# Performance work log

Measured on AMD Instinct MI355X. Metric: run time of the kernel, lower is better.

Reference implementation:

```python
import jax, jax.numpy as jnp
import numpy as np

B = 1024       # repertoires (batch)
TCR = 100      # instances (TCRs) per repertoire
FEAT = 15      # feature_num (conv in_channels)
AA = 24        # aa_num (sequence length)
KS = [2, 3, 4, 5, 6, 7]
FN = [3, 3, 3, 2, 2, 1]
NINP = 14      # sum(FN)
EPS = 1e-5     # BatchNorm eps


def sparsemax(z):
    # z: (B, K); sparsemax along axis 1 (Martins & Astudillo 2016)
    K = z.shape[1]
    zs = -jnp.sort(-z, axis=1)               # descending sort
    cs = jnp.cumsum(zs, axis=1)
    k = jnp.arange(1, K + 1, dtype=z.dtype)
    support = 1.0 + k * zs > cs              # (B, K) bool
    ksel = jnp.sum(support, axis=1, keepdims=True).astype(jnp.int32)  # support size
    tau = (jnp.take_along_axis(cs, ksel - 1, axis=1) - 1.0) / ksel.astype(z.dtype)
    return jnp.maximum(z - tau, 0.0)


def setup_inputs() -> dict:
    key = jax.random.key(0)
    ks = jax.random.split(key, 12)
    inp = {"x": jax.random.normal(ks[0], (B, TCR, FEAT, AA), dtype=jnp.float32)}
    for i, (h, f) in enumerate(zip(KS, FN)):
        inp[f"cw{i}"] = jax.random.normal(ks[1 + i], (f, FEAT, h), dtype=jnp.float32) * 0.1
        inp[f"cb{i}"] = jnp.zeros((f,), dtype=jnp.float32)
    inp["fc1_w"] = jax.random.normal(ks[7], (NINP, NINP), dtype=jnp.float32) * 0.2
    inp["fc1_b"] = jnp.zeros((NINP,), dtype=jnp.float32)
    inp["waout_w"] = jax.random.normal(ks[8], (1, NINP), dtype=jnp.float32) * 0.2
    inp["decf_w"] = jax.random.normal(ks[9], (NINP, NINP), dtype=jnp.float32) * 0.2
    inp["decf_b"] = jnp.zeros((NINP,), dtype=jnp.float32)
    inp["bn_g"] = jnp.ones((NINP,), dtype=jnp.float32)
    inp["bn_b"] = jnp.zeros((NINP,), dtype=jnp.float32)
    inp["decs_w"] = jax.random.normal(ks[10], (2, NINP), dtype=jnp.float32) * 0.2
    inp["decs_b"] = jnp.zeros((2,), dtype=jnp.float32)
    return inp


def reference(x, cw0, cb0, cw1, cb1, cw2, cb2, cw3, cb3, cw4, cb4, cw5, cb5,
              fc1_w, fc1_b, waout_w, decf_w, decf_b, bn_g, bn_b, decs_w, decs_b):
    xf = x.reshape(-1, FEAT, AA)  # (B*TCR, 15, 24)
    feats = []
    for w, b in ((cw0, cb0), (cw1, cb1), (cw2, cb2), (cw3, cb3), (cw4, cb4), (cw5, cb5)):
        y = jax.lax.conv_general_dilated(xf, w, (1,), 'VALID',
                                         dimension_numbers=('NCH', 'OIH', 'NCH'))
        y = jax.nn.relu(y + b[None, :, None])
        feats.append(jnp.max(y, axis=-1))  # AdaptiveMaxPool1d(1): global max over length
    out = jnp.concatenate(feats, axis=1).reshape(-1, TCR, NINP)  # (B, TCR, 14)
    # fclayer1 + dropout(eval=identity) + relu; applied per-instance so the
    # torch (TCR, B, .) transpose is equivalent to working in (B, TCR, .)
    h = jax.nn.relu(out @ fc1_w.T + fc1_b)                       # (B, TCR, 14)
    attw = sparsemax(h @ waout_w[0])                             # (B, TCR)
    pooled = jnp.einsum('bt,btd->bd', attw, h)                   # bmm(attw[:,None,:], h)
    z = pooled @ decf_w.T + decf_b                               # decoder_f
    mu = jnp.mean(z, axis=0)                                     # BatchNorm1d (batch stats)
    var = jnp.var(z, axis=0)
    z = jax.nn.relu((z - mu) / jnp.sqrt(var + EPS) * bn_g + bn_b)
    logits = z @ decs_w.T + decs_b                               # decoder_s -> (B, 2)
    return logits, attw
```

## Files before the change

kernel.cpp:

```cpp
#include <hip/hip_runtime.h>

typedef unsigned int  u32;
typedef unsigned short u16;

__device__ __forceinline__ float bf2f(u16 u){
    return __uint_as_float(((u32)u) << 16);
}
__device__ __forceinline__ float lo16(u32 v){ return __uint_as_float(v << 16); }
__device__ __forceinline__ float hi16(u32 v){ return __uint_as_float(v & 0xffff0000u); }
__device__ __forceinline__ u16 f2bf(float f){
    u32 x = __float_as_uint(f);
    x += 0x7fffu + ((x >> 16) & 1u);
    return (u16)(x >> 16);
}
__device__ __forceinline__ float ldany(const void* p, int i, bool bf){
    return bf ? bf2f(((const u16*)p)[i]) : ((const float*)p)[i];
}

#define B_      1024
#define TCR_    100
#define NINST   (B_*TCR_)

#define OFF_WCH    0
#define OFF_CB     840
#define OFF_FC1W   854
#define OFF_FC1B   1050
#define OFF_WA     1064
#define OFF_DECFW  1078
#define OFF_DECFB  1274
#define OFF_BNG    1288
#define OFF_BNB    1302
#define OFF_DECSW  1316
#define OFF_DECSB  1344

__global__ __launch_bounds__(256) void k_pack(
    const void* cw0, const void* cb0, const void* cw1, const void* cb1,
    const void* cw2, const void* cb2, const void* cw3, const void* cb3,
    const void* cw4, const void* cb4, const void* cw5, const void* cb5,
    const void* fc1_w, const void* fc1_b, const void* waout,
    const void* decf_w, const void* decf_b,
    const void* bn_g, const void* bn_b,
    const void* decs_w, const void* decs_b,
    float* __restrict__ wsP)
{
    const int tid = threadIdx.x;
    const bool bf = (((const u16*)bn_g)[0] == 0x3F80u);

    for (int widx = tid; widx < 840; widx += 256){
        float val; int dst;
        if (widx < 90)      { int e = widx;       int c=e/6,  rr=e-c*6,  ff=rr/2, j=rr-ff*2; val=ldany(cw0,(ff*15+c)*2+j,bf); dst=c*56+ 0+ff*2+j; }
        else if (widx < 225){ int e = widx - 90;  int c=e/9,  rr=e-c*9,  ff=rr/3, j=rr-ff*3; val=ldany(cw1,(ff*15+c)*3+j,bf); dst=c*56+ 6+ff*3+j; }
        else if (widx < 405){ int e = widx - 225; int c=e/12, rr=e-c*12, ff=rr/4, j=rr-ff*4; val=ldany(cw2,(ff*15+c)*4+j,bf); dst=c*56+15+ff*4+j; }
        else if (widx < 555){ int e = widx - 405; int c=e/10, rr=e-c*10, ff=rr/5, j=rr-ff*5; val=ldany(cw3,(ff*15+c)*5+j,bf); dst=c*56+27+ff*5+j; }
        else if (widx < 735){ int e = widx - 555; int c=e/12, rr=e-c*12, ff=rr/6, j=rr-ff*6; val=ldany(cw4,(ff*15+c)*6+j,bf); dst=c*56+37+ff*6+j; }
        else                { int e = widx - 735; int c=e/7,  j=e-c*7;                        val=ldany(cw5,c*7+j,bf);        dst=c*56+49+j; }
        wsP[OFF_WCH + dst] = val;
    }
    for (int i = tid; i < 14; i += 256){
        float bv;
        if (i < 3)       bv = ldany(cb0, i, bf);
        else if (i < 6)  bv = ldany(cb1, i - 3, bf);
        else if (i < 9)  bv = ldany(cb2, i - 6, bf);
        else if (i < 11) bv = ldany(cb3, i - 9, bf);
        else if (i < 13) bv = ldany(cb4, i - 11, bf);
        else             bv = ldany(cb5, 0, bf);
        wsP[OFF_CB    + i] = bv;
        wsP[OFF_FC1B  + i] = ldany(fc1_b,  i, bf);
        wsP[OFF_WA    + i] = ldany(waout,  i, bf);
        wsP[OFF_DECFB + i] = ldany(decf_b, i, bf);
        wsP[OFF_BNG   + i] = ldany(bn_g,   i, bf);
        wsP[OFF_BNB   + i] = ldany(bn_b,   i, bf);
    }
    for (int i = tid; i < 196; i += 256){
        wsP[OFF_FC1W  + i] = ldany(fc1_w,  i, bf);
        wsP[OFF_DECFW + i] = ldany(decf_w, i, bf);
    }
    for (int i = tid; i < 28; i += 256) wsP[OFF_DECSW + i] = ldany(decs_w, i, bf);
    for (int i = tid; i < 2;  i += 256) wsP[OFF_DECSB + i] = ldany(decs_b, i, bf);
}

template<int H, int F, int GOFF>
__device__ __forceinline__ void acc_ch(float (&acc)[F][17 - H], const float* xr,
                                       const float* __restrict__ wch){
    float wv[F * H];
    #pragma unroll
    for (int k = 0; k < F * H; ++k) wv[k] = wch[GOFF + k];
    #pragma unroll
    for (int ff = 0; ff < F; ++ff)
        #pragma unroll
        for (int i = 0; i < 17 - H; ++i)
            #pragma unroll
            for (int j = 0; j < H; ++j)
                acc[ff][i] = fmaf(wv[ff * H + j], xr[i + j], acc[ff][i]);
}

template<int H, int F, int OF>
__device__ __forceinline__ void pair_max(float (&acc)[F][17 - H],
                                         const float* __restrict__ wsP, float* feats){
    #pragma unroll
    for (int ff = 0; ff < F; ++ff){
        float m = acc[ff][0];
        #pragma unroll
        for (int i = 1; i < 17 - H; ++i) m = fmaxf(m, acc[ff][i]);
        m = fmaxf(m, __shfl_xor(m, 1));
        feats[OF + ff] = fmaxf(m + wsP[OFF_CB + OF + ff], 0.0f);
    }
}

template<bool BF>
__device__ __forceinline__ void unpack16(const uint4* buf, float* xr){
    if (BF){
        #pragma unroll
        for (int i = 0; i < 2; ++i){
            u32 w0 = buf[i].x, w1 = buf[i].y, w2 = buf[i].z, w3 = buf[i].w;
            xr[i*8+0] = lo16(w0); xr[i*8+1] = hi16(w0);
            xr[i*8+2] = lo16(w1); xr[i*8+3] = hi16(w1);
            xr[i*8+4] = lo16(w2); xr[i*8+5] = hi16(w2);
            xr[i*8+6] = lo16(w3); xr[i*8+7] = hi16(w3);
        }
    } else {
        #pragma unroll
        for (int i = 0; i < 4; ++i){
            xr[i*4+0] = __uint_as_float(buf[i].x);
            xr[i*4+1] = __uint_as_float(buf[i].y);
            xr[i*4+2] = __uint_as_float(buf[i].z);
            xr[i*4+3] = __uint_as_float(buf[i].w);
        }
    }
}

template<bool BF>
__device__ __forceinline__ void conv_body(const void* __restrict__ x,
                                          const float* __restrict__ wsP,
                                          float* __restrict__ hbufT,
                                          float* __restrict__ sbuf){
    constexpr int NB = BF ? 2 : 4;
    constexpr int CS = BF ? 48 : 96;
    const int tid   = threadIdx.x;
    const int tpart = tid & 1;
    const int inst  = blockIdx.x * 128 + (tid >> 1);
    const char* xb  = (const char*)x + (size_t)inst * (BF ? 720 : 1440)
                                     + tpart * (BF ? 16 : 32);

    float a2[3][15], a3[3][14], a4[3][13], a5[2][12], a6[2][11], a7[1][10];
    #pragma unroll
    for (int f = 0; f < 3; ++f){
        #pragma unroll
        for (int i = 0; i < 15; ++i) a2[f][i] = 0.0f;
        #pragma unroll
        for (int i = 0; i < 14; ++i) a3[f][i] = 0.0f;
        #pragma unroll
        for (int i = 0; i < 13; ++i) a4[f][i] = 0.0f;
    }
    #pragma unroll
    for (int f = 0; f < 2; ++f){
        #pragma unroll
        for (int i = 0; i < 12; ++i) a5[f][i] = 0.0f;
        #pragma unroll
        for (int i = 0; i < 11; ++i) a6[f][i] = 0.0f;
    }
    #pragma unroll
    for (int i = 0; i < 10; ++i) a7[0][i] = 0.0f;

    uint4 cur[NB];
    {
        const uint4* p = (const uint4*)xb;
        #pragma unroll
        for (int i = 0; i < NB; ++i) cur[i] = p[i];
    }
    #pragma unroll 1
    for (int c = 0; c < 15; ++c){
        uint4 nxt[NB];
        int cn = (c < 14) ? (c + 1) : 14;
        const uint4* pn = (const uint4*)(xb + cn * CS);
        #pragma unroll
        for (int i = 0; i < NB; ++i) nxt[i] = pn[i];

        float xr[16];
        unpack16<BF>(cur, xr);
        const float* wch = wsP + OFF_WCH + c * 56;
        acc_ch<2,3, 0>(a2, xr, wch);
        acc_ch<3,3, 6>(a3, xr, wch);
        acc_ch<4,3,15>(a4, xr, wch);
        acc_ch<5,2,27>(a5, xr, wch);
        acc_ch<6,2,37>(a6, xr, wch);
        acc_ch<7,1,49>(a7, xr, wch);

        #pragma unroll
        for (int i = 0; i < NB; ++i) cur[i] = nxt[i];
    }

    float feats[14];
    pair_max<2,3, 0>(a2, wsP, feats);
    pair_max<3,3, 3>(a3, wsP, feats);
    pair_max<4,3, 6>(a4, wsP, feats);
    pair_max<5,2, 9>(a5, wsP, feats);
    pair_max<6,2,11>(a6, wsP, feats);
    pair_max<7,1,13>(a7, wsP, feats);

    float hv[14];
    #pragma unroll
    for (int i = 0; i < 14; ++i){
        float a = wsP[OFF_FC1B + i];
        #pragma unroll
        for (int j = 0; j < 14; ++j) a = fmaf(feats[j], wsP[OFF_FC1W + i * 14 + j], a);
        hv[i] = fmaxf(a, 0.0f);
    }
    float sc = 0.0f;
    #pragma unroll
    for (int i = 0; i < 14; ++i) sc = fmaf(hv[i], wsP[OFF_WA + i], sc);

    if (tpart == 0){
        #pragma unroll
        for (int d = 0; d < 14; ++d) hbufT[d * NINST + inst] = hv[d];
        sbuf[inst] = sc;
    }
}

__global__ __launch_bounds__(256) void k_conv(
    const void* __restrict__ x, const float* __restrict__ wsP,
    const void* __restrict__ dt,
    float* __restrict__ hbufT, float* __restrict__ sbuf)
{
    const bool bf = (((const u16*)dt)[0] == 0x3F80u);
    if (bf) conv_body<true >(x, wsP, hbufT, sbuf);
    else    conv_body<false>(x, wsP, hbufT, sbuf);
}

__global__ __launch_bounds__(64) void k_sparse(
    const float* __restrict__ hbufT, const float* __restrict__ sbuf,
    const float* __restrict__ wsP, const void* __restrict__ dt,
    float* __restrict__ zbuf, void* __restrict__ d_out)
{
    const int b    = blockIdx.x;
    const int lane = threadIdx.x;
    const bool bf  = (((const u16*)dt)[0] == 0x3F80u);
    const bool has2 = lane < (TCR_ - 64);

    float z0 = sbuf[b * TCR_ + lane];
    float z1 = has2 ? sbuf[b * TCR_ + 64 + lane] : -1e30f;

    float m = fmaxf(z0, z1);
    #pragma unroll
    for (int o = 32; o; o >>= 1) m = fmaxf(m, __shfl_xor(m, o));

    float lo = m - 1.0f, hi = m;
    for (int it = 0; it < 32; ++it){
        float mid = 0.5f * (lo + hi);
        float s = fmaxf(z0 - mid, 0.0f) + fmaxf(z1 - mid, 0.0f);
        #pragma unroll
        for (int o = 32; o; o >>= 1) s += __shfl_xor(s, o);
        if (s >= 1.0f) lo = mid; else hi = mid;
    }
    float tau = 0.5f * (lo + hi);
    float a0 = fmaxf(z0 - tau, 0.0f);
    float a1 = fmaxf(z1 - tau, 0.0f);

    if (bf){
        u16* aw = (u16*)d_out + 2048;
        aw[b * TCR_ + lane] = f2bf(a0);
        if (has2) aw[b * TCR_ + 64 + lane] = f2bf(a1);
    } else {
        float* aw = (float*)d_out + 2048;
        aw[b * TCR_ + lane] = a0;
        if (has2) aw[b * TCR_ + 64 + lane] = a1;
    }

    float ap[14];
    #pragma unroll
    for (int d = 0; d < 14; ++d){
        float v = a0 * hbufT[d * NINST + b * TCR_ + lane];
        if (has2) v += a1 * hbufT[d * NINST + b * TCR_ + 64 + lane];
        #pragma unroll
        for (int o = 32; o; o >>= 1) v += __shfl_xor(v, o);
        ap[d] = v;
    }
    if (lane < 14){
        float zv = wsP[OFF_DECFB + lane];
        #pragma unroll
        for (int j = 0; j < 14; ++j) zv = fmaf(ap[j], wsP[OFF_DECFW + lane * 14 + j], zv);
        zbuf[b * 14 + lane] = zv;
    }
}

__global__ __launch_bounds__(256) void k_bn(
    const float* __restrict__ zbuf, const float* __restrict__ wsP,
    const void* __restrict__ dt, void* __restrict__ d_out)
{
    __shared__ float part[4][28];
    __shared__ float red[28];
    const int tid  = threadIdx.x;
    const int lane = tid & 63;
    const int w    = tid >> 6;
    const bool bf  = (((const u16*)dt)[0] == 0x3F80u);

    float z[4][14];
    #pragma unroll
    for (int r = 0; r < 4; ++r)
        #pragma unroll
        for (int d = 0; d < 14; ++d) z[r][d] = zbuf[(tid + 256 * r) * 14 + d];

    #pragma unroll
    for (int d = 0; d < 14; ++d){
        float s = 0.0f, q = 0.0f;
        #pragma unroll
        for (int r = 0; r < 4; ++r){ s += z[r][d]; q += z[r][d] * z[r][d]; }
        #pragma unroll
        for (int o = 32; o; o >>= 1){ s += __shfl_xor(s, o); q += __shfl_xor(q, o); }
        if (lane == 0){ part[w][d] = s; part[w][14 + d] = q; }
    }
    __syncthreads();
    if (tid < 28) red[tid] = part[0][tid] + part[1][tid] + part[2][tid] + part[3][tid];
    __syncthreads();

    float mu[14], rs[14];
    #pragma unroll
    for (int d = 0; d < 14; ++d){
        mu[d] = red[d] * (1.0f / 1024.0f);
        float var = red[14 + d] * (1.0f / 1024.0f) - mu[d] * mu[d];
        rs[d] = rsqrtf(var + 1e-5f);
    }
    #pragma unroll
    for (int r = 0; r < 4; ++r){
        float zn[14];
        #pragma unroll
        for (int d = 0; d < 14; ++d)
            zn[d] = fmaxf((z[r][d] - mu[d]) * rs[d] * wsP[OFF_BNG + d] + wsP[OFF_BNB + d], 0.0f);
        #pragma unroll
        for (int c = 0; c < 2; ++c){
            float a = wsP[OFF_DECSB + c];
            #pragma unroll
            for (int d = 0; d < 14; ++d) a = fmaf(zn[d], wsP[OFF_DECSW + c * 14 + d], a);
            if (bf) ((u16*)d_out)[(tid + 256 * r) * 2 + c] = f2bf(a);
            else    ((float*)d_out)[(tid + 256 * r) * 2 + c] = a;
        }
    }
}

extern "C" void kernel_launch(void* const* d_in, const int* in_sizes, int n_in,
                              void* d_out, int out_size, void* d_ws, size_t ws_size,
                              hipStream_t stream)
{
    (void)in_sizes; (void)n_in; (void)out_size; (void)ws_size;
    const void* x     = d_in[0];
    const void* bn_g  = d_in[18];

    float* wsP   = (float*)d_ws;
    float* hbufT = wsP + 2048;
    float* sbuf  = hbufT + (size_t)14 * NINST;
    float* zbuf  = sbuf + NINST;

    k_pack<<<1, 256, 0, stream>>>(
        d_in[1], d_in[2], d_in[3], d_in[4], d_in[5], d_in[6],
        d_in[7], d_in[8], d_in[9], d_in[10], d_in[11], d_in[12],
        d_in[13], d_in[14], d_in[15], d_in[16], d_in[17],
        d_in[18], d_in[19], d_in[20], d_in[21], wsP);
    k_conv<<<NINST / 128, 256, 0, stream>>>(x, wsP, bn_g, hbufT, sbuf);
    k_sparse<<<B_, 64, 0, stream>>>(hbufT, sbuf, wsP, bn_g, zbuf, d_out);
    k_bn<<<1, 256, 0, stream>>>(zbuf, wsP, bn_g, d_out);
}
```

Before: 302.5 us.

## Fuse BatchNorm into sparsemax kernel via last-block atomic, use DPP reductions

Removes the separate single-block BatchNorm/decoder kernel by having the last-finishing sparsemax block, detected with an atomic counter reset in the conv kernel, compute batch statistics and logits. Wave reductions switch from shfl_xor to DPP row/broadcast ops with a readlane, and the conv pair-max uses a quad-permute DPP. The sparsemax bisection drops from 32 to 16 iterations and then computes the exact tau from the support set. This saves one launch and shortens the serial reduction chains, at the cost of a tail where one wave does all of the BN work and a reliance on threadfence/atomic ordering.

```diff
diff --git a/kernel.cpp b/kernel.cpp
--- a/kernel.cpp
+++ b/kernel.cpp
@@ -32,6 +32,33 @@
 #define OFF_BNB    1302
 #define OFF_DECSW  1316
 #define OFF_DECSB  1344
+
+template<int CTRL, int RM, int BM, bool BC>
+__device__ __forceinline__ float dpp_mv(float old_, float x){
+    return __int_as_float(__builtin_amdgcn_update_dpp(
+        __float_as_int(old_), __float_as_int(x), CTRL, RM, BM, BC));
+}
+__device__ __forceinline__ float wave_sum_u(float x){
+    x += dpp_mv<0x111,0xf,0xf,true >(0.0f, x);
+    x += dpp_mv<0x112,0xf,0xf,true >(0.0f, x);
+    x += dpp_mv<0x114,0xf,0xf,true >(0.0f, x);
+    x += dpp_mv<0x118,0xf,0xf,true >(0.0f, x);
+    x += dpp_mv<0x142,0xa,0xf,true >(0.0f, x);
+    x += dpp_mv<0x143,0xc,0xf,true >(0.0f, x);
+    return __int_as_float(__builtin_amdgcn_readlane(__float_as_int(x), 63));
+}
+__device__ __forceinline__ float wave_max_u(float x){
+    x = fmaxf(x, dpp_mv<0x111,0xf,0xf,false>(x, x));
+    x = fmaxf(x, dpp_mv<0x112,0xf,0xf,false>(x, x));
+    x = fmaxf(x, dpp_mv<0x114,0xf,0xf,false>(x, x));
+    x = fmaxf(x, dpp_mv<0x118,0xf,0xf,false>(x, x));
+    x = fmaxf(x, dpp_mv<0x142,0xa,0xf,false>(x, x));
+    x = fmaxf(x, dpp_mv<0x143,0xc,0xf,false>(x, x));
+    return __int_as_float(__builtin_amdgcn_readlane(__float_as_int(x), 63));
+}
+__device__ __forceinline__ float qmax1(float m){
+    return fmaxf(m, dpp_mv<0xB1,0xf,0xf,false>(m, m));
+}
 
 __global__ __launch_bounds__(256) void k_pack(
     const void* cw0, const void* cb0, const void* cw1, const void* cb1,
@@ -102,7 +129,7 @@
         float m = acc[ff][0];
         #pragma unroll
         for (int i = 1; i < 17 - H; ++i) m = fmaxf(m, acc[ff][i]);
-        m = fmaxf(m, __shfl_xor(m, 1));
+        m = qmax1(m);
         feats[OF + ff] = fmaxf(m + wsP[OFF_CB + OF + ff], 0.0f);
     }
 }
@@ -133,7 +160,10 @@
 __device__ __forceinline__ void conv_body(const void* __restrict__ x,
                                           const float* __restrict__ wsP,
                                           float* __restrict__ hbufT,
-                                          float* __restrict__ sbuf){
+                                          float* __restrict__ sbuf,
+                                          unsigned* __restrict__ cnt){
+    if (blockIdx.x == 0 && threadIdx.x == 0) *cnt = 0u;
+
     constexpr int NB = BF ? 2 : 4;
     constexpr int CS = BF ? 48 : 96;
     const int tid   = threadIdx.x;
@@ -220,17 +250,19 @@
 __global__ __launch_bounds__(256) void k_conv(
     const void* __restrict__ x, const float* __restrict__ wsP,
     const void* __restrict__ dt,
-    float* __restrict__ hbufT, float* __restrict__ sbuf)
+    float* __restrict__ hbufT, float* __restrict__ sbuf,
+    unsigned* __restrict__ cnt)
 {
     const bool bf = (((const u16*)dt)[0] == 0x3F80u);
-    if (bf) conv_body<true >(x, wsP, hbufT, sbuf);
-    else    conv_body<false>(x, wsP, hbufT, sbuf);
-}
-
-__global__ __launch_bounds__(64) void k_sparse(
+    if (bf) conv_body<true >(x, wsP, hbufT, sbuf, cnt);
+    else    conv_body<false>(x, wsP, hbufT, sbuf, cnt);
+}
+
+__global__ __launch_bounds__(64) void k_sparse_fused(
     const float* __restrict__ hbufT, const float* __restrict__ sbuf,
     const float* __restrict__ wsP, const void* __restrict__ dt,
-    float* __restrict__ zbuf, void* __restrict__ d_out)
+    float* __restrict__ zbufT, unsigned* __restrict__ cnt,
+    void* __restrict__ d_out)
 {
     const int b    = blockIdx.x;
     const int lane = threadIdx.x;
@@ -240,19 +272,22 @@
     float z0 = sbuf[b * TCR_ + lane];
     float z1 = has2 ? sbuf[b * TCR_ + 64 + lane] : -1e30f;
 
-    float m = fmaxf(z0, z1);
-    #pragma unroll
-    for (int o = 32; o; o >>= 1) m = fmaxf(m, __shfl_xor(m, o));
+    float m = wave_max_u(fmaxf(z0, z1));
 
     float lo = m - 1.0f, hi = m;
-    for (int it = 0; it < 32; ++it){
+    #pragma unroll 1
+    for (int it = 0; it < 16; ++it){
         float mid = 0.5f * (lo + hi);
-        float s = fmaxf(z0 - mid, 0.0f) + fmaxf(z1 - mid, 0.0f);
-        #pragma unroll
-        for (int o = 32; o; o >>= 1) s += __shfl_xor(s, o);
+        float s = wave_sum_u(fmaxf(z0 - mid, 0.0f) + fmaxf(z1 - mid, 0.0f));
         if (s >= 1.0f) lo = mid; else hi = mid;
     }
-    float tau = 0.5f * (lo + hi);
+    float tm   = 0.5f * (lo + hi);
+    float i0   = (z0 > tm) ? 1.0f : 0.0f;
+    float i1   = (z1 > tm) ? 1.0f : 0.0f;
+    float ssum = wave_sum_u(i0 * z0 + i1 * z1);
+    float kcnt = wave_sum_u(i0 + i1);
+    float tau  = (ssum - 1.0f) / kcnt;
+
     float a0 = fmaxf(z0 - tau, 0.0f);
     float a1 = fmaxf(z1 - tau, 0.0f);
 
@@ -271,68 +306,59 @@
     for (int d = 0; d < 14; ++d){
         float v = a0 * hbufT[d * NINST + b * TCR_ + lane];
         if (has2) v += a1 * hbufT[d * NINST + b * TCR_ + 64 + lane];
-        #pragma unroll
-        for (int o = 32; o; o >>= 1) v += __shfl_xor(v, o);
-        ap[d] = v;
+        ap[d] = wave_sum_u(v);
     }
     if (lane < 14){
         float zv = wsP[OFF_DECFB + lane];
         #pragma unroll
         for (int j = 0; j < 14; ++j) zv = fmaf(ap[j], wsP[OFF_DECFW + lane * 14 + j], zv);
-        zbuf[b * 14 + lane] = zv;
-    }
-}
-
-__global__ __launch_bounds__(256) void k_bn(
-    const float* __restrict__ zbuf, const float* __restrict__ wsP,
-    const void* __restrict__ dt, void* __restrict__ d_out)
-{
-    __shared__ float part[4][28];
-    __shared__ float red[28];
-    const int tid  = threadIdx.x;
-    const int lane = tid & 63;
-    const int w    = tid >> 6;
-    const bool bf  = (((const u16*)dt)[0] == 0x3F80u);
-
-    float z[4][14];
-    #pragma unroll
-    for (int r = 0; r < 4; ++r)
-        #pragma unroll
-        for (int d = 0; d < 14; ++d) z[r][d] = zbuf[(tid + 256 * r) * 14 + d];
-
+        zbufT[lane * B_ + b] = zv;
+    }
+
+    __threadfence();
+    int old = 0;
+    if (lane == 0) old = (int)atomicAdd(cnt, 1u);
+    old = __shfl(old, 0);
+    if (old != (B_ - 1)) return;
+
+    __threadfence();
+    float mu[14], rs[14];
     #pragma unroll
     for (int d = 0; d < 14; ++d){
         float s = 0.0f, q = 0.0f;
         #pragma unroll
-        for (int r = 0; r < 4; ++r){ s += z[r][d]; q += z[r][d] * z[r][d]; }
-        #pragma unroll
-        for (int o = 32; o; o >>= 1){ s += __shfl_xor(s, o); q += __shfl_xor(q, o); }
-        if (lane == 0){ part[w][d] = s; part[w][14 + d] = q; }
-    }
-    __syncthreads();
-    if (tid < 28) red[tid] = part[0][tid] + part[1][tid] + part[2][tid] + part[3][tid];
-    __syncthreads();
-
-    float mu[14], rs[14];
+        for (int k = 0; k < 16; ++k){
+            float v = zbufT[d * B_ + lane + 64 * k];
+            s += v; q += v * v;
+        }
+        s = wave_sum_u(s); q = wave_sum_u(q);
+        float mm = s * (1.0f / 1024.0f);
+        mu[d] = mm;
+        rs[d] = rsqrtf(q * (1.0f / 1024.0f) - mm * mm + 1e-5f);
+    }
+    float g[14], bb[14], w0[14], w1[14];
     #pragma unroll
     for (int d = 0; d < 14; ++d){
-        mu[d] = red[d] * (1.0f / 1024.0f);
-        float var = red[14 + d] * (1.0f / 1024.0f) - mu[d] * mu[d];
-        rs[d] = rsqrtf(var + 1e-5f);
-    }
-    #pragma unroll
-    for (int r = 0; r < 4; ++r){
-        float zn[14];
-        #pragma unroll
-        for (int d = 0; d < 14; ++d)
-            zn[d] = fmaxf((z[r][d] - mu[d]) * rs[d] * wsP[OFF_BNG + d] + wsP[OFF_BNB + d], 0.0f);
-        #pragma unroll
-        for (int c = 0; c < 2; ++c){
-            float a = wsP[OFF_DECSB + c];
-            #pragma unroll
-            for (int d = 0; d < 14; ++d) a = fmaf(zn[d], wsP[OFF_DECSW + c * 14 + d], a);
-            if (bf) ((u16*)d_out)[(tid + 256 * r) * 2 + c] = f2bf(a);
-            else    ((float*)d_out)[(tid + 256 * r) * 2 + c] = a;
+        g[d]  = wsP[OFF_BNG + d];  bb[d] = wsP[OFF_BNB + d];
+        w0[d] = wsP[OFF_DECSW + d]; w1[d] = wsP[OFF_DECSW + 14 + d];
+    }
+    const float c0b = wsP[OFF_DECSB], c1b = wsP[OFF_DECSB + 1];
+    #pragma unroll
+    for (int k = 0; k < 16; ++k){
+        const int bi = lane + 64 * k;
+        float acc0 = c0b, acc1 = c1b;
+        #pragma unroll
+        for (int d = 0; d < 14; ++d){
+            float v  = zbufT[d * B_ + bi];
+            float zn = fmaxf((v - mu[d]) * rs[d] * g[d] + bb[d], 0.0f);
+            acc0 = fmaf(zn, w0[d], acc0);
+            acc1 = fmaf(zn, w1[d], acc1);
+        }
+        if (bf){
+            u32 pk = (u32)f2bf(acc0) | ((u32)f2bf(acc1) << 16);
+            ((u32*)d_out)[bi] = pk;
+        } else {
+            ((float2*)d_out)[bi] = make_float2(acc0, acc1);
         }
     }
 }
@@ -342,20 +368,20 @@
                               hipStream_t stream)
 {
     (void)in_sizes; (void)n_in; (void)out_size; (void)ws_size;
-    const void* x     = d_in[0];
-    const void* bn_g  = d_in[18];
-
-    float* wsP   = (float*)d_ws;
-    float* hbufT = wsP + 2048;
-    float* sbuf  = hbufT + (size_t)14 * NINST;
-    float* zbuf  = sbuf + NINST;
+    const void* x    = d_in[0];
+    const void* bn_g = d_in[18];
+
+    float* wsP    = (float*)d_ws;
+    float* hbufT  = wsP + 2048;
+    float* sbuf   = hbufT + (size_t)14 * NINST;
+    float* zbufT  = sbuf + NINST;
+    unsigned* cnt = (unsigned*)(zbufT + 14 * B_);
 
     k_pack<<<1, 256, 0, stream>>>(
         d_in[1], d_in[2], d_in[3], d_in[4], d_in[5], d_in[6],
         d_in[7], d_in[8], d_in[9], d_in[10], d_in[11], d_in[12],
         d_in[13], d_in[14], d_in[15], d_in[16], d_in[17],
         d_in[18], d_in[19], d_in[20], d_in[21], wsP);
-    k_conv<<<NINST / 128, 256, 0, stream>>>(x, wsP, bn_g, hbufT, sbuf);
-    k_sparse<<<B_, 64, 0, stream>>>(hbufT, sbuf, wsP, bn_g, zbuf, d_out);
-    k_bn<<<1, 256, 0, stream>>>(zbuf, wsP, bn_g, d_out);
-}
+    k_conv<<<NINST / 128, 256, 0, stream>>>(x, wsP, bn_g, hbufT, sbuf, cnt);
+    k_sparse_fused<<<B_, 64, 0, stream>>>(hbufT, sbuf, wsP, bn_g, zbufT, cnt, d_out);
+}
```

After: 319.5 us. +5.6%, slower.
